# Kernel optimization log

Measured on AMD Instinct MI355X. Metric: run time of the kernel, lower is better.

Reference implementation:

```python
import jax, jax.numpy as jnp
import numpy as np
from jax import lax

N = 50000
E = 320000
IN_DIM = 128
OUT_DIM = 64
N_CHANNEL = 8
KERNEL = 3
N_REL = 500
BN_EPS = 1e-5


def setup_inputs() -> dict:
    key = jax.random.key(0)
    ks = jax.random.split(key, 10)
    inp = jax.random.normal(ks[0], (N, IN_DIM), dtype=jnp.float32)
    heads = jax.random.randint(ks[1], (E,), 0, N)
    rels = jax.random.randint(ks[2], (E,), 0, N_REL)
    tails = jax.random.randint(ks[3], (E,), 0, N)
    triple = jnp.stack([heads, rels, tails], axis=1).astype(jnp.int64)
    # parameters
    limit_W = float(np.sqrt(6.0 / (IN_DIM + OUT_DIM)))  # xavier_uniform
    W = jax.random.uniform(ks[4], (IN_DIM, OUT_DIM), minval=-limit_W, maxval=limit_W, dtype=jnp.float32)
    rel_embed = jax.random.normal(ks[5], (N_REL, OUT_DIM), dtype=jnp.float32)
    fan_in = 1 * KERNEL * KERNEL
    b = float(1.0 / np.sqrt(fan_in))
    conv_w = jax.random.uniform(ks[6], (N_CHANNEL, 1, KERNEL, KERNEL), minval=-b, maxval=b, dtype=jnp.float32)
    conv_b = jax.random.uniform(ks[7], (N_CHANNEL,), minval=-b, maxval=b, dtype=jnp.float32)
    fc_in = N_CHANNEL * (OUT_DIM - KERNEL + 1) * (3 - KERNEL + 1)
    bf = float(1.0 / np.sqrt(fc_in))
    fc_w = jax.random.uniform(ks[8], (1, fc_in), minval=-bf, maxval=bf, dtype=jnp.float32)
    bn1_gamma = jnp.ones((1,), jnp.float32)
    bn1_beta = jnp.zeros((1,), jnp.float32)
    bn2_gamma = jnp.ones((N_CHANNEL,), jnp.float32)
    bn2_beta = jnp.zeros((N_CHANNEL,), jnp.float32)
    return {"input": inp, "triple": triple, "W": W, "rel_embed": rel_embed,
            "conv_w": conv_w, "conv_b": conv_b, "fc_w": fc_w,
            "bn1_gamma": bn1_gamma, "bn1_beta": bn1_beta,
            "bn2_gamma": bn2_gamma, "bn2_beta": bn2_beta}


def _bn_eval(x, gamma, beta):
    # eval-mode BatchNorm with running_mean=0, running_var=1
    scale = gamma / jnp.sqrt(1.0 + BN_EPS)
    return x * scale.reshape(1, -1, 1, 1) + beta.reshape(1, -1, 1, 1)


def reference(input, triple, W, rel_embed, conv_w, conv_b, fc_w,
              bn1_gamma, bn1_beta, bn2_gamma, bn2_beta):
    n = input.shape[0]
    inp = input @ W                       # [N, out_dim]
    head = triple[:, 0]
    tail = triple[:, 2]
    h = inp[head]                         # [E, D]
    r = rel_embed[triple[:, 1]]           # [E, D]
    t = inp[tail]                         # [E, D]
    # energy function: [E,1,D,3] -> bn1 -> conv -> bn2 -> relu -> fc
    x = jnp.stack([h, r, t], axis=-1)[:, None, :, :]   # [E,1,D,3]
    x = _bn_eval(x, bn1_gamma, bn1_beta)
    y = lax.conv_general_dilated(x, conv_w, (1, 1), 'VALID',
                                 dimension_numbers=('NCHW', 'OIHW', 'NCHW'))
    y = y + conv_b.reshape(1, -1, 1, 1)                 # [E,C,D-2,1]
    y = jax.nn.relu(_bn_eval(y, bn2_gamma, bn2_beta))
    y = y.reshape(y.shape[0], -1)
    e = y @ fc_w[0]                                     # [E]
    e = jax.nn.leaky_relu(e, 0.01)
    # sparse softmax over rows (head) then sparse mm with input_
    m = jax.ops.segment_max(e, head, num_segments=n)
    ex = jnp.exp(e - m[head])
    denom = jax.ops.segment_sum(ex, head, num_segments=n)
    attn = ex / denom[head]
    agg = jax.ops.segment_sum(attn[:, None] * t, head, num_segments=n)
    return jax.nn.elu(agg + inp)
```

## Files before the change

kernel.cpp:

```cpp
#include <hip/hip_runtime.h>
#include <hip/hip_bf16.h>
#include <stdint.h>

#define IN_DIM   128
#define OUT_DIM  64
#define NCH      8
#define N_REL    500
#define BN_EPS   1e-5f
#define CAP      32


__device__ __forceinline__ void fold_cw_thread(
    const float* __restrict__ conv_w, const float* __restrict__ conv_b,
    const float* __restrict__ bn1g, const float* __restrict__ bn1b,
    const float* __restrict__ bn2g, const float* __restrict__ bn2b,
    float* __restrict__ cw, int c)
{
    if (c >= NCH) return;
    float rs  = rsqrtf(1.f + BN_EPS);
    float s1  = bn1g[0] * rs;
    float be1 = bn1b[0];
    float s2  = bn2g[c] * rs;
    float k1  = s1 * s2;
    float wsum = 0.f;
    for (int d = 0; d < 3; ++d) {
        float a  = conv_w[c * 9 + d * 3 + 0];
        float b  = conv_w[c * 9 + d * 3 + 1];
        float cc = conv_w[c * 9 + d * 3 + 2];
        wsum += a + b + cc;
        cw[c * 3 + d]      = k1 * a;
        cw[24 + c * 3 + d] = k1 * b;
        cw[48 + c * 3 + d] = k1 * cc;
    }
    cw[72 + c] = (be1 * wsum + conv_b[c]) * s2 + bn2b[c];
}

__global__ __launch_bounds__(256) void k_build(
    const float* __restrict__ X, const float* __restrict__ W,
    const int* __restrict__ triple,
    const float* __restrict__ conv_w, const float* __restrict__ conv_b,
    const float* __restrict__ bn1g, const float* __restrict__ bn1b,
    const float* __restrict__ bn2g, const float* __restrict__ bn2b,
    float* __restrict__ inp, int* __restrict__ cnt, int2* __restrict__ rt32,
    float* __restrict__ cw, int E, int N)
{
    const int gtid    = blockIdx.x * 256 + threadIdx.x;
    const int gstride = gridDim.x * 256;

    if (blockIdx.x == 0 && threadIdx.x < NCH)
        fold_cw_thread(conv_w, conv_b, bn1g, bn1b, bn2g, bn2b, cw, threadIdx.x);

    const int wv = __builtin_amdgcn_readfirstlane(threadIdx.x >> 6);
    const int ln = threadIdx.x & 63;
    const int ntiles = (N + 31) / 32;
    for (int tile = blockIdx.x; tile < ntiles; tile += gridDim.x) {
        const int rows0 = tile * 32 + wv * 8;
        float acc[8];
        #pragma unroll
        for (int r = 0; r < 8; ++r) acc[r] = 0.f;
        #pragma unroll 2
        for (int k4 = 0; k4 < IN_DIM / 4; ++k4) {
            const int k = k4 * 4;
            float w0 = W[(k + 0) * OUT_DIM + ln];
            float w1 = W[(k + 1) * OUT_DIM + ln];
            float w2 = W[(k + 2) * OUT_DIM + ln];
            float w3 = W[(k + 3) * OUT_DIM + ln];
            #pragma unroll
            for (int r = 0; r < 8; ++r) {
                const int row = min(rows0 + r, N - 1);
                const float4 x = *(const float4*)(X + (unsigned)row * IN_DIM + k);
                acc[r] = fmaf(x.w, w3, fmaf(x.z, w2, fmaf(x.y, w1, fmaf(x.x, w0, acc[r]))));
            }
        }
        #pragma unroll
        for (int r = 0; r < 8; ++r) {
            const int row = rows0 + r;
            if (row < N) inp[(unsigned)row * OUT_DIM + ln] = acc[r];
        }
    }

    for (int j = gtid; j < E; j += gstride) {
        int h = triple[3 * j], r = triple[3 * j + 1], t = triple[3 * j + 2];
        h = min(max(h, 0), N - 1);
        r = min(max(r, 0), N_REL - 1);
        t = min(max(t, 0), N - 1);
        int pos = atomicAdd(&cnt[h], 1);
        if (pos < CAP) rt32[(unsigned)h * CAP + pos] = make_int2(r, t);
    }
}

__device__ __forceinline__ float dpp_wave_sum(float x) {
    x += __int_as_float(__builtin_amdgcn_update_dpp(0, __float_as_int(x), 0x111, 0xf, 0xf, true));
    x += __int_as_float(__builtin_amdgcn_update_dpp(0, __float_as_int(x), 0x112, 0xf, 0xf, true));
    x += __int_as_float(__builtin_amdgcn_update_dpp(0, __float_as_int(x), 0x114, 0xf, 0xf, true));
    x += __int_as_float(__builtin_amdgcn_update_dpp(0, __float_as_int(x), 0x118, 0xf, 0xf, true));
    x += __int_as_float(__builtin_amdgcn_update_dpp(0, __float_as_int(x), 0x142, 0xf, 0xf, true));
    x += __int_as_float(__builtin_amdgcn_update_dpp(0, __float_as_int(x), 0x143, 0xf, 0xf, true));
    return __int_as_float(__builtin_amdgcn_readlane(__float_as_int(x), 63));
}

__global__ __launch_bounds__(256, 4) void k_fused_all(
    const float* __restrict__ inp, const float* __restrict__ rel_embed,
    const float* __restrict__ cw, const float* __restrict__ fc_w,
    const int* __restrict__ cnt, const int2* __restrict__ rt32,
    float* __restrict__ out, int N)
{
    const int lane   = threadIdx.x & 63;
    const int wave   = (blockIdx.x * (blockDim.x >> 6)) + (threadIdx.x >> 6);
    const int nwaves = gridDim.x * (blockDim.x >> 6);

    float fcl[NCH];
    #pragma unroll
    for (int c = 0; c < NCH; ++c)
        fcl[c] = (lane < 62) ? fc_w[c * 62 + lane] : 0.f;

    for (int h = wave; h < N; h += nwaves) {
        const int deg = min(cnt[h], CAP);

        float h0 = inp[(unsigned)h * OUT_DIM + lane];
        float h1 = __shfl_down(h0, 1, 64), h2 = __shfl_down(h0, 2, 64);
        float Ht[NCH];
        #pragma unroll
        for (int c = 0; c < NCH; ++c) {
            float v = cw[72 + c];
            v = fmaf(cw[c * 3 + 0], h0, v);
            v = fmaf(cw[c * 3 + 1], h1, v);
            v = fmaf(cw[c * 3 + 2], h2, v);
            Ht[c] = v;
        }

        float m_run = -INFINITY, l_run = 0.f, agg = 0.f;
        int2 rtv = make_int2(0, 0);
        if (lane < deg) rtv = rt32[(unsigned)h * CAP + lane];

        if (deg > 0) {
            int rk = __builtin_amdgcn_readlane(rtv.x, 0);
            int tk = __builtin_amdgcn_readlane(rtv.y, 0);
            float rr = rel_embed[(unsigned)rk * OUT_DIM + lane];
            float tt = inp      [(unsigned)tk * OUT_DIM + lane];

            for (int k = 0; k < deg; ++k) {
                float rrN = 0.f, ttN = 0.f;
                if (k + 1 < deg) {
                    int rk1 = __builtin_amdgcn_readlane(rtv.x, k + 1);
                    int tk1 = __builtin_amdgcn_readlane(rtv.y, k + 1);
                    rrN = rel_embed[(unsigned)rk1 * OUT_DIM + lane];
                    ttN = inp      [(unsigned)tk1 * OUT_DIM + lane];
                }
                float r1 = __shfl_down(rr, 1, 64), r2 = __shfl_down(rr, 2, 64);
                float t1 = __shfl_down(tt, 1, 64), t2 = __shfl_down(tt, 2, 64);

                float acc = 0.f;
                #pragma unroll
                for (int c = 0; c < NCH; ++c) {
                    float y = Ht[c];
                    y = fmaf(cw[24 + c * 3 + 0], rr, y);
                    y = fmaf(cw[24 + c * 3 + 1], r1, y);
                    y = fmaf(cw[24 + c * 3 + 2], r2, y);
                    y = fmaf(cw[48 + c * 3 + 0], tt, y);
                    y = fmaf(cw[48 + c * 3 + 1], t1, y);
                    y = fmaf(cw[48 + c * 3 + 2], t2, y);
                    acc = fmaf(fmaxf(y, 0.f), fcl[c], acc);
                }
                float s  = dpp_wave_sum(acc);
                float ev = fmaxf(s, 0.01f * s);

                float mn = fmaxf(m_run, ev);
                float sc = __expf(m_run - mn);
                float wk = __expf(ev - mn);
                agg   = fmaf(agg, sc, wk * tt);
                l_run = fmaf(l_run, sc, wk);
                m_run = mn;

                rr = rrN; tt = ttN;
            }
        }
        float aggn = (l_run > 0.f) ? agg / l_run : 0.f;
        float x = aggn + h0;
        float y = x > 0.f ? x : (__expf(x) - 1.f);
        out[(unsigned)h * OUT_DIM + lane] = y;
    }
}

extern "C" void kernel_launch(void* const* d_in, const int* in_sizes, int n_in,
                              void* d_out, int out_size, void* d_ws, size_t ws_size,
                              hipStream_t stream)
{
    const float* input     = (const float*)d_in[0];
    const int*   triple    = (const int*)d_in[1];
    const float* W         = (const float*)d_in[2];
    const float* rel_embed = (const float*)d_in[3];
    const float* conv_w    = (const float*)d_in[4];
    const float* conv_b    = (const float*)d_in[5];
    const float* fc_w      = (const float*)d_in[6];
    const float* bn1g      = (const float*)d_in[7];
    const float* bn1b      = (const float*)d_in[8];
    const float* bn2g      = (const float*)d_in[9];
    const float* bn2b      = (const float*)d_in[10];
    float*       out       = (float*)d_out;

    const int N = in_sizes[0] / IN_DIM;
    const int E = in_sizes[1] / 3;

    auto align = [](size_t x) { return (x + 255) & ~(size_t)255; };
    char* base = (char*)d_ws;
    size_t o = 0;
    float* inp  = (float*)(base + o); o = align(o + (size_t)N * OUT_DIM * 4);
    int2*  rt32 = (int2*)(base + o);  o = align(o + (size_t)N * CAP * 8);
    float* cw   = (float*)(base + o); o = align(o + 80 * 4);
    int*   cnt  = (int*)(base + o);   o = align(o + (size_t)N * 4);

    hipMemsetAsync(cnt, 0, (size_t)N * 4, stream);

    k_build<<<1024, 256, 0, stream>>>(
        input, W, triple, conv_w, conv_b, bn1g, bn1b, bn2g, bn2b,
        inp, cnt, rt32, cw, E, N);
    k_fused_all<<<4096, 256, 0, stream>>>(inp, rel_embed, cw, fc_w,
                                          cnt, rt32, out, N);
}
```

Before: 200.5 us.

## Stage W and X tiles in LDS; use DPP shifts in fused attention loop

The projection GEMM in k_build now copies all of W into shared memory once per block and stages 16-row tiles of X in LDS, so each wave computes 4 rows from LDS rather than re-reading global memory. In the fused attention kernel, the cross-lane shuffles (__shfl_down by 1 and 2) become chained DPP wave_shl1 moves, which avoids LDS-based permutes in the hot per-edge loop. The next-edge prefetch no longer has a branch, since lanes past the degree hold index 0 and always point at a valid row. Empty asm keep-alive constraints pin fcl and Ht in registers; the cost is extra barriers and 40 KB of LDS per block in k_build.

```diff
diff --git a/kernel.cpp b/kernel.cpp
--- a/kernel.cpp
+++ b/kernel.cpp
@@ -8,7 +8,15 @@
 #define N_REL    500
 #define BN_EPS   1e-5f
 #define CAP      32
-
+#define TILE_ROWS 16
+
+
+#define KEEP(x) asm volatile("" : "+v"(x))
+
+__device__ __forceinline__ float dpp_shl1(float x) {
+    return __int_as_float(__builtin_amdgcn_update_dpp(
+        0, __float_as_int(x), 0x130, 0xf, 0xf, true));
+}
 
 __device__ __forceinline__ void fold_cw_thread(
     const float* __restrict__ conv_w, const float* __restrict__ conv_b,
@@ -44,39 +52,48 @@
     float* __restrict__ inp, int* __restrict__ cnt, int2* __restrict__ rt32,
     float* __restrict__ cw, int E, int N)
 {
+    __shared__ float Wl[IN_DIM * OUT_DIM];
+    __shared__ float Xl[TILE_ROWS * IN_DIM];
     const int gtid    = blockIdx.x * 256 + threadIdx.x;
     const int gstride = gridDim.x * 256;
 
     if (blockIdx.x == 0 && threadIdx.x < NCH)
         fold_cw_thread(conv_w, conv_b, bn1g, bn1b, bn2g, bn2b, cw, threadIdx.x);
 
-    const int wv = __builtin_amdgcn_readfirstlane(threadIdx.x >> 6);
-    const int ln = threadIdx.x & 63;
-    const int ntiles = (N + 31) / 32;
+    for (int i = threadIdx.x; i < IN_DIM * OUT_DIM / 4; i += 256)
+        ((float4*)Wl)[i] = ((const float4*)W)[i];
+    __syncthreads();
+    const int wv = threadIdx.x >> 6, ln = threadIdx.x & 63;
+    const int ntiles = (N + TILE_ROWS - 1) / TILE_ROWS;
     for (int tile = blockIdx.x; tile < ntiles; tile += gridDim.x) {
-        const int rows0 = tile * 32 + wv * 8;
-        float acc[8];
-        #pragma unroll
-        for (int r = 0; r < 8; ++r) acc[r] = 0.f;
-        #pragma unroll 2
+        const int rows0 = tile * TILE_ROWS;
+        for (int i = threadIdx.x; i < TILE_ROWS * IN_DIM / 4; i += 256) {
+            int r = i >> 5, k4 = i & 31;
+            int rr = rows0 + r;
+            float4 v = make_float4(0.f, 0.f, 0.f, 0.f);
+            if (rr < N) v = ((const float4*)X)[(unsigned)rr * (IN_DIM / 4) + k4];
+            ((float4*)Xl)[i] = v;
+        }
+        __syncthreads();
+        float acc[4] = {0.f, 0.f, 0.f, 0.f};
         for (int k4 = 0; k4 < IN_DIM / 4; ++k4) {
-            const int k = k4 * 4;
-            float w0 = W[(k + 0) * OUT_DIM + ln];
-            float w1 = W[(k + 1) * OUT_DIM + ln];
-            float w2 = W[(k + 2) * OUT_DIM + ln];
-            float w3 = W[(k + 3) * OUT_DIM + ln];
+            int k = k4 * 4;
+            float w0 = Wl[(k + 0) * OUT_DIM + ln];
+            float w1 = Wl[(k + 1) * OUT_DIM + ln];
+            float w2 = Wl[(k + 2) * OUT_DIM + ln];
+            float w3 = Wl[(k + 3) * OUT_DIM + ln];
             #pragma unroll
-            for (int r = 0; r < 8; ++r) {
-                const int row = min(rows0 + r, N - 1);
-                const float4 x = *(const float4*)(X + (unsigned)row * IN_DIM + k);
+            for (int r = 0; r < 4; ++r) {
+                const float4 x = *(const float4*)&Xl[(wv * 4 + r) * IN_DIM + k];
                 acc[r] = fmaf(x.w, w3, fmaf(x.z, w2, fmaf(x.y, w1, fmaf(x.x, w0, acc[r]))));
             }
         }
         #pragma unroll
-        for (int r = 0; r < 8; ++r) {
-            const int row = rows0 + r;
+        for (int r = 0; r < 4; ++r) {
+            int row = rows0 + wv * 4 + r;
             if (row < N) inp[(unsigned)row * OUT_DIM + ln] = acc[r];
         }
+        __syncthreads();
     }
 
     for (int j = gtid; j < E; j += gstride) {
@@ -111,14 +128,17 @@
 
     float fcl[NCH];
     #pragma unroll
-    for (int c = 0; c < NCH; ++c)
+    for (int c = 0; c < NCH; ++c) {
         fcl[c] = (lane < 62) ? fc_w[c * 62 + lane] : 0.f;
+        KEEP(fcl[c]);
+    }
 
     for (int h = wave; h < N; h += nwaves) {
         const int deg = min(cnt[h], CAP);
 
         float h0 = inp[(unsigned)h * OUT_DIM + lane];
-        float h1 = __shfl_down(h0, 1, 64), h2 = __shfl_down(h0, 2, 64);
+        float h1 = dpp_shl1(h0);
+        float h2 = dpp_shl1(h1);
         float Ht[NCH];
         #pragma unroll
         for (int c = 0; c < NCH; ++c) {
@@ -127,6 +147,7 @@
             v = fmaf(cw[c * 3 + 1], h1, v);
             v = fmaf(cw[c * 3 + 2], h2, v);
             Ht[c] = v;
+            KEEP(Ht[c]);
         }
 
         float m_run = -INFINITY, l_run = 0.f, agg = 0.f;
@@ -140,15 +161,13 @@
             float tt = inp      [(unsigned)tk * OUT_DIM + lane];
 
             for (int k = 0; k < deg; ++k) {
-                float rrN = 0.f, ttN = 0.f;
-                if (k + 1 < deg) {
-                    int rk1 = __builtin_amdgcn_readlane(rtv.x, k + 1);
-                    int tk1 = __builtin_amdgcn_readlane(rtv.y, k + 1);
-                    rrN = rel_embed[(unsigned)rk1 * OUT_DIM + lane];
-                    ttN = inp      [(unsigned)tk1 * OUT_DIM + lane];
-                }
-                float r1 = __shfl_down(rr, 1, 64), r2 = __shfl_down(rr, 2, 64);
-                float t1 = __shfl_down(tt, 1, 64), t2 = __shfl_down(tt, 2, 64);
+                int rk1 = __builtin_amdgcn_readlane(rtv.x, k + 1);
+                int tk1 = __builtin_amdgcn_readlane(rtv.y, k + 1);
+                float rrN = rel_embed[(unsigned)rk1 * OUT_DIM + lane];
+                float ttN = inp      [(unsigned)tk1 * OUT_DIM + lane];
+
+                float r1 = dpp_shl1(rr), r2 = dpp_shl1(r1);
+                float t1 = dpp_shl1(tt), t2 = dpp_shl1(t1);
 
                 float acc = 0.f;
                 #pragma unroll
```

Result: slower. 356.8 us (+77.9%).
